# Performance work log

Measured on AMD Instinct MI355X. Metric: run time of the kernel, lower is better.

Reference implementation:

```python
import jax, jax.numpy as jnp
import numpy as np

B, L, F_DIM, H = 4, 384, 640, 128
K_COULOMB = 332.0
DIELECTRIC = 80.0
BN_EPS = 1e-5

# amino-acid charge table, index order 'ACDEFGHIKLMNPQRSTVWY'
_AA = 'ACDEFGHIKLMNPQRSTVWY'
_CHG = {'D': -1.0, 'E': -1.0, 'K': 1.0, 'R': 1.0, 'H': 0.1}
_TABLE = np.zeros((20, 3), dtype=np.float32)
for _i, _aa in enumerate(_AA):
    c = _CHG.get(_aa, 0.0)
    _TABLE[_i, 0 if c > 0 else (1 if c < 0 else 2)] = 1.0
CHG_TABLE = jnp.asarray(_TABLE)


def _conv1d(x, w, b, pad):
    # x: [N, Cin, L], w: [Cout, Cin, K]
    y = jax.lax.conv_general_dilated(x, w, (1,), [(pad, pad)],
                                     dimension_numbers=('NCH', 'OIH', 'NCH'))
    return y + b[None, :, None]


def setup_inputs() -> dict:
    key = jax.random.key(0)
    ks = jax.random.split(key, 32)
    s = 0.05

    def rn(k, shape):
        return (jax.random.normal(k, shape) * s).astype(jnp.float32)

    inp = {
        'features': jax.random.normal(ks[0], (B, L, F_DIM), dtype=jnp.float32),
        'seq_ids': jax.random.randint(ks[1], (B, L), 0, 20, dtype=jnp.int32),
        'structures': (jax.random.normal(ks[2], (B, L, 3)) * 10.0).astype(jnp.float32),
        # charge predictor: Linear(F,H) -> ReLU -> BN(H) -> Linear(H,H//2) -> ReLU -> Linear(H//2,3) -> Softmax
        'W1': rn(ks[3], (F_DIM, H)), 'b1': jnp.zeros((H,), jnp.float32),
        'gamma': jnp.ones((H,), jnp.float32), 'beta': jnp.zeros((H,), jnp.float32),
        'rmean': jnp.zeros((H,), jnp.float32), 'rvar': jnp.ones((H,), jnp.float32),
        'W2': rn(ks[4], (H, H // 2)), 'b2': jnp.zeros((H // 2,), jnp.float32),
        'W3': rn(ks[5], (H // 2, 3)), 'b3': jnp.zeros((3,), jnp.float32),
        # salt bridge detector: Linear(2F+1,H) -> ReLU -> Linear(H,64) -> ReLU -> Linear(64,1) -> Sigmoid
        'sW1': rn(ks[6], (2 * F_DIM + 1, H)), 'sb1': jnp.zeros((H,), jnp.float32),
        'sW2': rn(ks[7], (H, 64)), 'sb2': jnp.zeros((64,), jnp.float32),
        'sW3': rn(ks[8], (64, 1)), 'sb3': jnp.zeros((1,), jnp.float32),
        # potential calculator convs (OIH layout)
        'c1w': rn(ks[9], (16, 1, 5)), 'c1b': jnp.zeros((16,), jnp.float32),
        'c2w': rn(ks[10], (8, 16, 3)), 'c2b': jnp.zeros((8,), jnp.float32),
        'c3w': rn(ks[11], (1, 8, 3)), 'c3b': jnp.zeros((1,), jnp.float32),
    }
    return inp


def reference(features, seq_ids, structures,
              W1, b1, gamma, beta, rmean, rvar, W2, b2, W3, b3,
              sW1, sb1, sW2, sb2, sW3, sb3,
              c1w, c1b, c2w, c2b, c3w, c3b):
    b_, l_, f_ = features.shape

    # true charges from sequence (one-hot pos/neg/neutral)
    true_charges = CHG_TABLE[seq_ids]                               # [B,L,3]

    # --- charge predictor (BatchNorm in eval mode: running stats) ---
    x = features.reshape(-1, f_)
    h = jax.nn.relu(x @ W1 + b1)
    h = gamma * (h - rmean) / jnp.sqrt(rvar + BN_EPS) + beta
    h = jax.nn.relu(h @ W2 + b2)
    pc = jax.nn.softmax(h @ W3 + b3, axis=-1).reshape(b_, l_, 3)    # [B,L,3]

    net_charge = pc[:, :, 0:1] - pc[:, :, 1:2]                      # [B,L,1]

    # --- electrostatic potential: 1D conv stack on [B,1,L] ---
    p = net_charge.transpose(0, 2, 1)                               # [B,1,L]
    p = jax.nn.relu(_conv1d(p, c1w, c1b, 2))
    p = jax.nn.relu(_conv1d(p, c2w, c2b, 1))
    p = _conv1d(p, c3w, c3b, 1)
    potential = p.transpose(0, 2, 1)                                # [B,L,1]

    # --- pairwise distances ---
    diff = structures[:, :, None, :] - structures[:, None, :, :]    # [B,L,L,3]
    D = jnp.sqrt(jnp.sum(diff * diff, axis=-1) + 1e-12)             # [B,L,L]

    # --- salt bridges: vectorized edge-MLP over all (pos i, neg j) pairs ---
    pos = pc[:, :, 0] > pc[:, :, 2]                                 # [B,L]
    neg = pc[:, :, 1] > pc[:, :, 2]                                 # [B,L]
    a, bb, d = sW1[:f_], sW1[f_:2 * f_], sW1[2 * f_]                # split cat([fi,fj,dist]) @ sW1
    fi = features @ a                                               # [B,L,H]
    fj = features @ bb                                              # [B,L,H]
    hid = jax.nn.relu(fi[:, :, None, :] + fj[:, None, :, :] + D[..., None] * d + sb1)  # [B,L,L,H]
    hid2 = jax.nn.relu(hid @ sW2 + sb2)                             # [B,L,L,64]
    prob = jax.nn.sigmoid((hid2 @ sW3 + sb3)[..., 0])               # [B,L,L]
    q = pos[:, :, None] & neg[:, None, :] & (D < 4.0) & (prob > 0.5)
    salt_bridge_masks = (q | q.transpose(0, 2, 1)).astype(jnp.float32)  # [B,L,L]

    # --- Coulomb energy with distance-dependent dielectric ---
    # dielectric = eps * D / 4 -> e_ij = k * q_i q_j / (eps/4 * D^2)
    qc = pc[:, :, 0] - pc[:, :, 1]                                  # [B,L]
    valid = (D < 15.0) & (D > 0.0)
    triu = jnp.triu(jnp.ones((l_, l_), bool), k=1)[None]
    D_safe = jnp.where(valid, D, 1.0)
    e_ij = K_COULOMB * qc[:, :, None] * qc[:, None, :] / ((DIELECTRIC / 4.0) * D_safe * D_safe)
    energy = jnp.sum(jnp.where(valid & triu, e_ij, 0.0), axis=(1, 2))  # [B]

    return (pc, true_charges, net_charge, potential, salt_bridge_masks, energy)
```

## Files before the change

### kernel.cpp

```cpp
#include <hip/hip_runtime.h>

#define LSEQ 384
#define NROWS 1536
#define FDIM 640
#define HDIM 128
#define PART 196608

#define WS_H1P 0
#define WS_FIP (4*PART)
#define WS_FJP (8*PART)
#define WS_FI  (12*PART)
#define WS_FJ  (13*PART)
#define WS_QC  (14*PART)
#define WS_FLAG (WS_QC + NROWS)

#define OUT_PC    0
#define OUT_TC    4608
#define OUT_NET   9216
#define OUT_POT   10752
#define OUT_MASK  12288
#define OUT_EN    602112

__global__ __launch_bounds__(256) void k_gemm(const float* __restrict__ X,
                                              const float* __restrict__ W1,
                                              const float* __restrict__ sW1,
                                              float* __restrict__ ws,
                                              float* __restrict__ out) {
    __shared__ float As[2 * 32 * 34];
    __shared__ float Bs[2 * 32 * 64];
    const int t = threadIdx.x;
    if (blockIdx.x == 0 && blockIdx.y == 0 && blockIdx.z == 0 && t < 4)
        out[OUT_EN + t] = 0.0f;

    const int m0 = blockIdx.x * 32;
    const int gy = blockIdx.y, kz = blockIdx.z;
    const int mat = gy >> 1, half = gy & 1, n0 = half * 64;
    const float* W = (mat == 0) ? W1 : (mat == 1 ? sW1 : sW1 + 640 * 128);
    float* O = ws + (mat == 0 ? WS_H1P : (mat == 1 ? WS_FIP : WS_FJP)) + kz * PART;

    const int a_r = t >> 3, a_c = (t & 7) * 4;
    const int b_r = t >> 4, b_c = (t & 15) * 4;
    const int tx = (t & 15) * 4, ty = (t >> 4) * 2;
    const int k0 = kz * 160;

    float acc[2][4] = {};

    float4 av  = *(const float4*)&X[(m0 + a_r) * FDIM + k0 + a_c];
    float4 bv0 = *(const float4*)&W[(k0 + b_r) * HDIM + n0 + b_c];
    float4 bv1 = *(const float4*)&W[(k0 + b_r + 16) * HDIM + n0 + b_c];
    As[(a_c + 0) * 34 + a_r] = av.x;
    As[(a_c + 1) * 34 + a_r] = av.y;
    As[(a_c + 2) * 34 + a_r] = av.z;
    As[(a_c + 3) * 34 + a_r] = av.w;
    *(float4*)&Bs[b_r * 64 + b_c]        = bv0;
    *(float4*)&Bs[(b_r + 16) * 64 + b_c] = bv1;
    __syncthreads();

    for (int it = 0; it < 5; it++) {
        const int buf = it & 1;
        if (it < 4) {
            const int kk = k0 + (it + 1) * 32;
            av  = *(const float4*)&X[(m0 + a_r) * FDIM + kk + a_c];
            bv0 = *(const float4*)&W[(kk + b_r) * HDIM + n0 + b_c];
            bv1 = *(const float4*)&W[(kk + b_r + 16) * HDIM + n0 + b_c];
        }
        const float* Ab = As + buf * 1088;
        const float* Bb = Bs + buf * 2048;
#pragma unroll
        for (int k = 0; k < 32; k++) {
            float2 a = *(const float2*)&Ab[k * 34 + ty];
            float4 b = *(const float4*)&Bb[k * 64 + tx];
            acc[0][0] = fmaf(a.x, b.x, acc[0][0]);
            acc[0][1] = fmaf(a.x, b.y, acc[0][1]);
            acc[0][2] = fmaf(a.x, b.z, acc[0][2]);
            acc[0][3] = fmaf(a.x, b.w, acc[0][3]);
            acc[1][0] = fmaf(a.y, b.x, acc[1][0]);
            acc[1][1] = fmaf(a.y, b.y, acc[1][1]);
            acc[1][2] = fmaf(a.y, b.z, acc[1][2]);
            acc[1][3] = fmaf(a.y, b.w, acc[1][3]);
        }
        if (it < 4) {
            float* Aw = As + (buf ^ 1) * 1088;
            float* Bw = Bs + (buf ^ 1) * 2048;
            Aw[(a_c + 0) * 34 + a_r] = av.x;
            Aw[(a_c + 1) * 34 + a_r] = av.y;
            Aw[(a_c + 2) * 34 + a_r] = av.z;
            Aw[(a_c + 3) * 34 + a_r] = av.w;
            *(float4*)&Bw[b_r * 64 + b_c]        = bv0;
            *(float4*)&Bw[(b_r + 16) * 64 + b_c] = bv1;
            __syncthreads();
        }
    }
#pragma unroll
    for (int r = 0; r < 2; r++) {
        float4 v = make_float4(acc[r][0], acc[r][1], acc[r][2], acc[r][3]);
        *(float4*)&O[(m0 + ty + r) * HDIM + n0 + tx] = v;
    }
}

__global__ __launch_bounds__(256) void k_row(float* __restrict__ ws,
                                             const float* __restrict__ b1,
                                             const float* __restrict__ gam,
                                             const float* __restrict__ bet,
                                             const float* __restrict__ rmean,
                                             const float* __restrict__ rvar,
                                             const float* __restrict__ W2,
                                             const float* __restrict__ b2,
                                             const float* __restrict__ W3,
                                             const float* __restrict__ b3,
                                             const int* __restrict__ seq,
                                             float* __restrict__ out) {
    const int t = threadIdx.x, w = t >> 6, lane = t & 63;
    const int row = blockIdx.x * 4 + w;
    const long base = (long)row * 128;
    const float* h1p = ws + WS_H1P;
    const float* fip = ws + WS_FIP;
    const float* fjp = ws + WS_FJP;

    {
        float fi0 = fip[base + lane] + fip[PART + base + lane]
                  + fip[2 * PART + base + lane] + fip[3 * PART + base + lane];
        float fi1 = fip[base + 64 + lane] + fip[PART + base + 64 + lane]
                  + fip[2 * PART + base + 64 + lane] + fip[3 * PART + base + 64 + lane];
        float fj0 = fjp[base + lane] + fjp[PART + base + lane]
                  + fjp[2 * PART + base + lane] + fjp[3 * PART + base + lane];
        float fj1 = fjp[base + 64 + lane] + fjp[PART + base + 64 + lane]
                  + fjp[2 * PART + base + 64 + lane] + fjp[3 * PART + base + 64 + lane];
        ws[WS_FI + base + lane]      = fi0;
        ws[WS_FI + base + 64 + lane] = fi1;
        ws[WS_FJ + base + lane]      = fj0;
        ws[WS_FJ + base + 64 + lane] = fj1;
    }

    float h0 = h1p[base + lane] + h1p[PART + base + lane]
             + h1p[2 * PART + base + lane] + h1p[3 * PART + base + lane];
    float h1 = h1p[base + 64 + lane] + h1p[PART + base + 64 + lane]
             + h1p[2 * PART + base + 64 + lane] + h1p[3 * PART + base + 64 + lane];
    h0 = fmaxf(h0 + b1[lane], 0.0f);
    h1 = fmaxf(h1 + b1[64 + lane], 0.0f);
    h0 = gam[lane]      * (h0 - rmean[lane])      / sqrtf(rvar[lane] + 1e-5f)      + bet[lane];
    h1 = gam[64 + lane] * (h1 - rmean[64 + lane]) / sqrtf(rvar[64 + lane] + 1e-5f) + bet[64 + lane];

    float acc = b2[lane];
#pragma unroll
    for (int cc = 0; cc < 64; cc++) {
        float wv0 = W2[cc * 64 + lane];
        float wv1 = W2[(cc + 64) * 64 + lane];
        float hv0 = __uint_as_float(__builtin_amdgcn_readlane(__float_as_uint(h0), cc));
        float hv1 = __uint_as_float(__builtin_amdgcn_readlane(__float_as_uint(h1), cc));
        acc = fmaf(hv0, wv0, acc);
        acc = fmaf(hv1, wv1, acc);
    }
    float h2 = fmaxf(acc, 0.0f);
    float x0 = h2 * W3[lane * 3 + 0];
    float x1 = h2 * W3[lane * 3 + 1];
    float x2 = h2 * W3[lane * 3 + 2];
#pragma unroll
    for (int o = 32; o > 0; o >>= 1) {
        x0 += __shfl_xor(x0, o, 64);
        x1 += __shfl_xor(x1, o, 64);
        x2 += __shfl_xor(x2, o, 64);
    }
    if (lane == 0) {
        float l0 = x0 + b3[0], l1 = x1 + b3[1], l2 = x2 + b3[2];
        float m = fmaxf(l0, fmaxf(l1, l2));
        float e0 = expf(l0 - m), e1 = expf(l1 - m), e2 = expf(l2 - m);
        float s = e0 + e1 + e2;
        float pc0 = e0 / s, pc1 = e1 / s, pc2 = e2 / s;
        out[OUT_PC + row * 3 + 0] = pc0;
        out[OUT_PC + row * 3 + 1] = pc1;
        out[OUT_PC + row * 3 + 2] = pc2;
        float net = pc0 - pc1;
        out[OUT_NET + row] = net;
        ws[WS_QC + row] = net;
        ((int*)(ws + WS_FLAG))[row] = (pc0 > pc2 ? 1 : 0) | (pc1 > pc2 ? 2 : 0);
        int sid = seq[row];
        float c0 = (sid == 6 || sid == 8 || sid == 14) ? 1.0f : 0.0f;
        float c1 = (sid == 2 || sid == 3) ? 1.0f : 0.0f;
        out[OUT_TC + row * 3 + 0] = c0;
        out[OUT_TC + row * 3 + 1] = c1;
        out[OUT_TC + row * 3 + 2] = (c0 == 0.0f && c1 == 0.0f) ? 1.0f : 0.0f;
    }
}

__device__ __forceinline__ float mlp_eval(const float* __restrict__ fi, const float* __restrict__ fj,
                                          int gi, int gj, float D,
                                          float dv0, float dv1, float sb0, float sb1v,
                                          float b2v, float w3l, const float* w2s, int lane) {
    float fi0 = fi[(long)gi * 128 + lane];
    float fi1 = fi[(long)gi * 128 + 64 + lane];
    float fj0 = fj[(long)gj * 128 + lane];
    float fj1 = fj[(long)gj * 128 + 64 + lane];
    float h0 = fmaxf(fi0 + fj0 + D * dv0 + sb0, 0.0f);
    float h1 = fmaxf(fi1 + fj1 + D * dv1 + sb1v, 0.0f);
    float a0 = 0.0f, a1 = 0.0f;
#pragma unroll
    for (int cc = 0; cc < 64; cc++) {
        float hv0 = __uint_as_float(__builtin_amdgcn_readlane(__float_as_uint(h0), cc));
        float hv1 = __uint_as_float(__builtin_amdgcn_readlane(__float_as_uint(h1), cc));
        a0 = fmaf(hv0, w2s[cc * 64 + lane], a0);
        a1 = fmaf(hv1, w2s[(cc + 64) * 64 + lane], a1);
    }
    float x = fmaxf(a0 + a1 + b2v, 0.0f) * w3l;
#pragma unroll
    for (int o = 32; o > 0; o >>= 1) x += __shfl_xor(x, o, 64);
    return x;
}

__global__ __launch_bounds__(256) void k2(const float* __restrict__ S,
                                          const float* __restrict__ ws,
                                          const float* __restrict__ sW1,
                                          const float* __restrict__ sb1,
                                          const float* __restrict__ sW2,
                                          const float* __restrict__ sb2,
                                          const float* __restrict__ sW3,
                                          const float* __restrict__ sb3,
                                          const float* __restrict__ c1w, const float* __restrict__ c1b,
                                          const float* __restrict__ c2w, const float* __restrict__ c2b,
                                          const float* __restrict__ c3w, const float* __restrict__ c3b,
                                          float* __restrict__ out) {
    __shared__ char smem[40960];
    const int t = threadIdx.x;
    const int bi = blockIdx.x;

    if (bi < 4) {
        float* p0 = (float*)smem;
        float* p1 = p0 + 388;
        float* p2 = p1 + 16 * 386;
        const int b = bi;
        for (int j = t; j < LSEQ; j += 256) p0[j + 2] = out[OUT_NET + b * LSEQ + j];
        if (t < 2) { p0[t] = 0.0f; p0[LSEQ + 2 + t] = 0.0f; }
        if (t < 16) { p1[t * 386] = 0.0f; p1[t * 386 + 385] = 0.0f; }
        if (t < 8)  { p2[t * 386] = 0.0f; p2[t * 386 + 385] = 0.0f; }
        __syncthreads();
        for (int pos = t; pos < LSEQ; pos += 256) {
#pragma unroll
            for (int o = 0; o < 16; o++) {
                float acc = c1b[o];
#pragma unroll
                for (int k = 0; k < 5; k++) acc = fmaf(p0[pos + k], c1w[o * 5 + k], acc);
                p1[o * 386 + pos + 1] = fmaxf(acc, 0.0f);
            }
        }
        __syncthreads();
        for (int pos = t; pos < LSEQ; pos += 256) {
#pragma unroll
            for (int o = 0; o < 8; o++) {
                float acc = c2b[o];
                for (int i = 0; i < 16; i++)
#pragma unroll
                    for (int k = 0; k < 3; k++)
                        acc = fmaf(p1[i * 386 + pos + k], c2w[(o * 16 + i) * 3 + k], acc);
                p2[o * 386 + pos + 1] = fmaxf(acc, 0.0f);
            }
        }
        __syncthreads();
        for (int pos = t; pos < LSEQ; pos += 256) {
            float acc = c3b[0];
            for (int i = 0; i < 8; i++)
#pragma unroll
                for (int k = 0; k < 3; k++)
                    acc = fmaf(p2[i * 386 + pos + k], c3w[i * 3 + k], acc);
            out[OUT_POT + b * LSEQ + pos] = acc;
        }
        return;
    }

    float* sx = (float*)smem;
    float* sy = sx + 384;
    float* sz = sy + 384;
    float* sq = sz + 384;
    unsigned int* clist = (unsigned int*)(sz + 768);
    unsigned char* sf = (unsigned char*)(smem + 7680);
    float* red = (float*)(smem + 8064);
    int* cntL = (int*)(smem + 8080);
    float* w2s = (float*)(smem + 8192);

    const float* qc = ws + WS_QC;
    const int* flags = (const int*)(ws + WS_FLAG);
    const float* fi = ws + WS_FI;
    const float* fj = ws + WS_FJ;

    const int row = bi - 4;
    const int b = row / LSEQ;
    const int i = row - b * LSEQ;

    for (int j = t; j < LSEQ; j += 256) {
        int g = b * LSEQ + j;
        sx[j] = S[g * 3 + 0];
        sy[j] = S[g * 3 + 1];
        sz[j] = S[g * 3 + 2];
        sq[j] = qc[g];
        sf[j] = (unsigned char)flags[g];
    }
    if (t == 0) *cntL = 0;
    __syncthreads();

    const float six = sx[i], siy = sy[i], siz = sz[i], qi = sq[i];
    const int fli = sf[i];
    const bool posi = (fli & 1) != 0, negi = (fli & 2) != 0;
    const int lane = t & 63, w = t >> 6;
    float esum = 0.0f;
    float* mrow = out + OUT_MASK + (long)row * LSEQ;

    for (int j = t; j < LSEQ; j += 256) {
        float dx = __fsub_rn(six, sx[j]);
        float dy = __fsub_rn(siy, sy[j]);
        float dz = __fsub_rn(siz, sz[j]);
        float d2 = __fadd_rn(__fadd_rn(__fmul_rn(dx, dx), __fmul_rn(dy, dy)), __fmul_rn(dz, dz));
        d2 = __fadd_rn(d2, 1e-12f);
        float D = __fsqrt_rn(d2);
        mrow[j] = 0.0f;
        if (j > i && D < 15.0f && D > 0.0f) {
            float num = __fmul_rn(__fmul_rn(332.0f, qi), sq[j]);
            float den = __fmul_rn(__fmul_rn(20.0f, D), D);
            esum += __fdiv_rn(num, den);
        }
        int flj = sf[j];
        bool near = (D < 4.0f);
        bool need1 = near && posi && ((flj & 2) != 0);
        bool need2 = near && negi && ((flj & 1) != 0);
        if (need1 || need2) {
            int p = atomicAdd(cntL, 1);
            clist[p] = (unsigned int)j | (need1 ? 512u : 0u) | (need2 ? 1024u : 0u);
        }
    }
#pragma unroll
    for (int o = 32; o > 0; o >>= 1) esum += __shfl_xor(esum, o, 64);
    if (lane == 0) red[w] = esum;
    __syncthreads();
    if (t == 0) {
        float s = red[0] + red[1] + red[2] + red[3];
        atomicAdd(&out[OUT_EN + b], s);
    }

    int nc = *cntL;
    if (nc == 0) return;

    for (int idx = t; idx < 2048; idx += 256)
        ((float4*)w2s)[idx] = ((const float4*)sW2)[idx];
    const float* dvec = sW1 + 1280 * 128;
    const float dv0 = dvec[lane], dv1 = dvec[lane + 64];
    const float sb0 = sb1[lane], sb1v = sb1[lane + 64];
    const float w3l = sW3[lane];
    const float b2v = sb2[lane];
    const float b3v = sb3[0];
    __syncthreads();

    for (int c = w; c < nc; c += 4) {
        unsigned int e = clist[c];
        int j = (int)(e & 511u);
        bool need1 = (e & 512u) != 0, need2 = (e & 1024u) != 0;
        float dx = __fsub_rn(six, sx[j]);
        float dy = __fsub_rn(siy, sy[j]);
        float dz = __fsub_rn(siz, sz[j]);
        float d2 = __fadd_rn(__fadd_rn(__fmul_rn(dx, dx), __fmul_rn(dy, dy)), __fmul_rn(dz, dz));
        d2 = __fadd_rn(d2, 1e-12f);
        float D = __fsqrt_rn(d2);
        int gi = row, gj = b * LSEQ + j;
        bool hit = false;
        if (need1) {
            float x = mlp_eval(fi, fj, gi, gj, D, dv0, dv1, sb0, sb1v, b2v, w3l, w2s, lane);
            hit = (x + b3v) > 0.0f;
        }
        if (!hit && need2) {
            float x = mlp_eval(fi, fj, gj, gi, D, dv0, dv1, sb0, sb1v, b2v, w3l, w2s, lane);
            hit = (x + b3v) > 0.0f;
        }
        if (hit && lane == 0) mrow[j] = 1.0f;
    }
}

extern "C" void kernel_launch(void* const* d_in, const int* in_sizes, int n_in,
                              void* d_out, int out_size, void* d_ws, size_t ws_size,
                              hipStream_t stream) {
    const float* X     = (const float*)d_in[0];
    const int*   seq   = (const int*)d_in[1];
    const float* S     = (const float*)d_in[2];
    const float* W1    = (const float*)d_in[3];
    const float* b1    = (const float*)d_in[4];
    const float* gam   = (const float*)d_in[5];
    const float* bet   = (const float*)d_in[6];
    const float* rmean = (const float*)d_in[7];
    const float* rvar  = (const float*)d_in[8];
    const float* W2    = (const float*)d_in[9];
    const float* b2    = (const float*)d_in[10];
    const float* W3    = (const float*)d_in[11];
    const float* b3    = (const float*)d_in[12];
    const float* sW1   = (const float*)d_in[13];
    const float* sb1   = (const float*)d_in[14];
    const float* sW2   = (const float*)d_in[15];
    const float* sb2   = (const float*)d_in[16];
    const float* sW3   = (const float*)d_in[17];
    const float* sb3   = (const float*)d_in[18];
    const float* c1w   = (const float*)d_in[19];
    const float* c1b   = (const float*)d_in[20];
    const float* c2w   = (const float*)d_in[21];
    const float* c2b   = (const float*)d_in[22];
    const float* c3w   = (const float*)d_in[23];
    const float* c3b   = (const float*)d_in[24];

    float* out = (float*)d_out;
    float* ws  = (float*)d_ws;

    hipLaunchKernelGGL(k_gemm, dim3(48, 6, 4), dim3(256), 0, stream, X, W1, sW1, ws, out);
    hipLaunchKernelGGL(k_row, dim3(384), dim3(256), 0, stream,
                       ws, b1, gam, bet, rmean, rvar, W2, b2, W3, b3, seq, out);
    hipLaunchKernelGGL(k2, dim3(1540), dim3(256), 0, stream,
                       S, ws, sW1, sb1, sW2, sb2, sW3, sb3,
                       c1w, c1b, c2w, c2b, c3w, c3b, out);
}
```

Measured before the change: 155.8 us.

## Shrink k2 shared memory, fuse conv chain in registers, spread energy reduction

Cuts k2's shared memory from 40KB to 8KB. The salt-bridge MLP now reads sW2 straight from global/L2 instead of staging it in LDS, and the launch bounds hint 6 blocks per CU to raise occupancy. The three potential convolutions are fused per position into register computation, recomputing the conv1 and conv2 halos instead of keeping intermediate LDS buffers. Energy accumulation now spreads atomics over 96 partial slots per batch, and the last block to finish does the final reduction. This avoids contended atomics on four output words but adds a completion counter and the cost of global-memory weight reads.

New measurement: 168.7 us. 8.3% more time.

```diff
diff --git a/kernel.cpp b/kernel.cpp
--- a/kernel.cpp
+++ b/kernel.cpp
@@ -13,6 +13,8 @@
 #define WS_FJ  (13*PART)
 #define WS_QC  (14*PART)
 #define WS_FLAG (WS_QC + NROWS)
+#define WS_EPART (WS_FLAG + NROWS)
+#define WS_DONE  (WS_EPART + 384)
 
 #define OUT_PC    0
 #define OUT_TC    4608
@@ -24,13 +26,14 @@
 __global__ __launch_bounds__(256) void k_gemm(const float* __restrict__ X,
                                               const float* __restrict__ W1,
                                               const float* __restrict__ sW1,
-                                              float* __restrict__ ws,
-                                              float* __restrict__ out) {
+                                              float* __restrict__ ws) {
     __shared__ float As[2 * 32 * 34];
     __shared__ float Bs[2 * 32 * 64];
     const int t = threadIdx.x;
-    if (blockIdx.x == 0 && blockIdx.y == 0 && blockIdx.z == 0 && t < 4)
-        out[OUT_EN + t] = 0.0f;
+    if (blockIdx.x == 0 && blockIdx.y == 0 && blockIdx.z == 0) {
+        for (int idx = t; idx < 385; idx += 256)
+            ws[WS_EPART + idx] = 0.0f;
+    }
 
     const int m0 = blockIdx.x * 32;
     const int gy = blockIdx.y, kz = blockIdx.z;
@@ -186,20 +189,16 @@
 __device__ __forceinline__ float mlp_eval(const float* __restrict__ fi, const float* __restrict__ fj,
                                           int gi, int gj, float D,
                                           float dv0, float dv1, float sb0, float sb1v,
-                                          float b2v, float w3l, const float* w2s, int lane) {
-    float fi0 = fi[(long)gi * 128 + lane];
-    float fi1 = fi[(long)gi * 128 + 64 + lane];
-    float fj0 = fj[(long)gj * 128 + lane];
-    float fj1 = fj[(long)gj * 128 + 64 + lane];
-    float h0 = fmaxf(fi0 + fj0 + D * dv0 + sb0, 0.0f);
-    float h1 = fmaxf(fi1 + fj1 + D * dv1 + sb1v, 0.0f);
+                                          float b2v, float w3l, const float* __restrict__ sW2, int lane) {
+    float h0 = fmaxf(fi[(long)gi * 128 + lane]      + fj[(long)gj * 128 + lane]      + D * dv0 + sb0,  0.0f);
+    float h1 = fmaxf(fi[(long)gi * 128 + 64 + lane] + fj[(long)gj * 128 + 64 + lane] + D * dv1 + sb1v, 0.0f);
     float a0 = 0.0f, a1 = 0.0f;
-#pragma unroll
+#pragma unroll 8
     for (int cc = 0; cc < 64; cc++) {
         float hv0 = __uint_as_float(__builtin_amdgcn_readlane(__float_as_uint(h0), cc));
         float hv1 = __uint_as_float(__builtin_amdgcn_readlane(__float_as_uint(h1), cc));
-        a0 = fmaf(hv0, w2s[cc * 64 + lane], a0);
-        a1 = fmaf(hv1, w2s[(cc + 64) * 64 + lane], a1);
+        a0 = fmaf(hv0, sW2[cc * 64 + lane], a0);
+        a1 = fmaf(hv1, sW2[(cc + 64) * 64 + lane], a1);
     }
     float x = fmaxf(a0 + a1 + b2v, 0.0f) * w3l;
 #pragma unroll
@@ -207,61 +206,68 @@
     return x;
 }
 
-__global__ __launch_bounds__(256) void k2(const float* __restrict__ S,
-                                          const float* __restrict__ ws,
-                                          const float* __restrict__ sW1,
-                                          const float* __restrict__ sb1,
-                                          const float* __restrict__ sW2,
-                                          const float* __restrict__ sb2,
-                                          const float* __restrict__ sW3,
-                                          const float* __restrict__ sb3,
-                                          const float* __restrict__ c1w, const float* __restrict__ c1b,
-                                          const float* __restrict__ c2w, const float* __restrict__ c2b,
-                                          const float* __restrict__ c3w, const float* __restrict__ c3b,
-                                          float* __restrict__ out) {
-    __shared__ char smem[40960];
+__global__ __launch_bounds__(256, 6) void k2(const float* __restrict__ S,
+                                             float* __restrict__ ws,
+                                             const float* __restrict__ sW1,
+                                             const float* __restrict__ sb1,
+                                             const float* __restrict__ sW2,
+                                             const float* __restrict__ sb2,
+                                             const float* __restrict__ sW3,
+                                             const float* __restrict__ sb3,
+                                             const float* __restrict__ c1w, const float* __restrict__ c1b,
+                                             const float* __restrict__ c2w, const float* __restrict__ c2b,
+                                             const float* __restrict__ c3w, const float* __restrict__ c3b,
+                                             float* __restrict__ out) {
+    __shared__ char smem[8192];
     const int t = threadIdx.x;
     const int bi = blockIdx.x;
 
     if (bi < 4) {
-        float* p0 = (float*)smem;
-        float* p1 = p0 + 388;
-        float* p2 = p1 + 16 * 386;
+        float* p0h = (float*)smem;
         const int b = bi;
-        for (int j = t; j < LSEQ; j += 256) p0[j + 2] = out[OUT_NET + b * LSEQ + j];
-        if (t < 2) { p0[t] = 0.0f; p0[LSEQ + 2 + t] = 0.0f; }
-        if (t < 16) { p1[t * 386] = 0.0f; p1[t * 386 + 385] = 0.0f; }
-        if (t < 8)  { p2[t * 386] = 0.0f; p2[t * 386 + 385] = 0.0f; }
+        for (int idx = t; idx < 392; idx += 256)
+            p0h[idx] = (idx >= 4 && idx < 388) ? out[OUT_NET + b * LSEQ + (idx - 4)] : 0.0f;
         __syncthreads();
         for (int pos = t; pos < LSEQ; pos += 256) {
-#pragma unroll
-            for (int o = 0; o < 16; o++) {
-                float acc = c1b[o];
-#pragma unroll
-                for (int k = 0; k < 5; k++) acc = fmaf(p0[pos + k], c1w[o * 5 + k], acc);
-                p1[o * 386 + pos + 1] = fmaxf(acc, 0.0f);
-            }
-        }
-        __syncthreads();
-        for (int pos = t; pos < LSEQ; pos += 256) {
-#pragma unroll
-            for (int o = 0; o < 8; o++) {
-                float acc = c2b[o];
-                for (int i = 0; i < 16; i++)
-#pragma unroll
-                    for (int k = 0; k < 3; k++)
-                        acc = fmaf(p1[i * 386 + pos + k], c2w[(o * 16 + i) * 3 + k], acc);
-                p2[o * 386 + pos + 1] = fmaxf(acc, 0.0f);
-            }
-        }
-        __syncthreads();
-        for (int pos = t; pos < LSEQ; pos += 256) {
-            float acc = c3b[0];
-            for (int i = 0; i < 8; i++)
-#pragma unroll
-                for (int k = 0; k < 3; k++)
-                    acc = fmaf(p2[i * 386 + pos + k], c3w[i * 3 + k], acc);
-            out[OUT_POT + b * LSEQ + pos] = acc;
+            float p2v[8][3];
+#pragma unroll
+            for (int o2 = 0; o2 < 8; o2++) {
+                float cb = c2b[o2];
+#pragma unroll
+                for (int d1 = 0; d1 < 3; d1++) p2v[o2][d1] = cb;
+            }
+            for (int i = 0; i < 16; i++) {
+                float p1v[5];
+#pragma unroll
+                for (int d2 = 0; d2 < 5; d2++) {
+                    int q2 = pos - 2 + d2;
+                    float a = c1b[i];
+#pragma unroll
+                    for (int k = 0; k < 5; k++)
+                        a = fmaf(p0h[q2 + 2 + k], c1w[i * 5 + k], a);
+                    p1v[d2] = (q2 >= 0 && q2 < LSEQ) ? fmaxf(a, 0.0f) : 0.0f;
+                }
+#pragma unroll
+                for (int o2 = 0; o2 < 8; o2++) {
+#pragma unroll
+                    for (int d1 = 0; d1 < 3; d1++) {
+#pragma unroll
+                        for (int k = 0; k < 3; k++)
+                            p2v[o2][d1] = fmaf(p1v[d1 + k], c2w[(o2 * 16 + i) * 3 + k], p2v[o2][d1]);
+                    }
+                }
+            }
+            float acc3 = c3b[0];
+#pragma unroll
+            for (int o2 = 0; o2 < 8; o2++) {
+#pragma unroll
+                for (int k = 0; k < 3; k++) {
+                    int q1 = pos - 1 + k;
+                    float pv = (q1 >= 0 && q1 < LSEQ) ? fmaxf(p2v[o2][k], 0.0f) : 0.0f;
+                    acc3 = fmaf(pv, c3w[o2 * 3 + k], acc3);
+                }
+            }
+            out[OUT_POT + b * LSEQ + pos] = acc3;
         }
         return;
     }
@@ -270,11 +276,10 @@
     float* sy = sx + 384;
     float* sz = sy + 384;
     float* sq = sz + 384;
-    unsigned int* clist = (unsigned int*)(sz + 768);
+    unsigned int* clist = (unsigned int*)(sq + 384);
     unsigned char* sf = (unsigned char*)(smem + 7680);
     float* red = (float*)(smem + 8064);
     int* cntL = (int*)(smem + 8080);
-    float* w2s = (float*)(smem + 8192);
 
     const float* qc = ws + WS_QC;
     const int* flags = (const int*)(ws + WS_FLAG);
@@ -329,45 +334,59 @@
     for (int o = 32; o > 0; o >>= 1) esum += __shfl_xor(esum, o, 64);
     if (lane == 0) red[w] = esum;
     __syncthreads();
+
+    int nc = *cntL;
+    float blockE = red[0] + red[1] + red[2] + red[3];
+
+    if (nc > 0) {
+        const float* dvec = sW1 + 1280 * 128;
+        const float dv0 = dvec[lane], dv1 = dvec[lane + 64];
+        const float sb0 = sb1[lane], sb1v = sb1[lane + 64];
+        const float w3l = sW3[lane];
+        const float b2v = sb2[lane];
+        const float b3v = sb3[0];
+        for (int c = w; c < nc; c += 4) {
+            unsigned int e = clist[c];
+            int j = (int)(e & 511u);
+            bool need1 = (e & 512u) != 0, need2 = (e & 1024u) != 0;
+            float dx = __fsub_rn(six, sx[j]);
+            float dy = __fsub_rn(siy, sy[j]);
+            float dz = __fsub_rn(siz, sz[j]);
+            float d2 = __fadd_rn(__fadd_rn(__fmul_rn(dx, dx), __fmul_rn(dy, dy)), __fmul_rn(dz, dz));
+            d2 = __fadd_rn(d2, 1e-12f);
+            float D = __fsqrt_rn(d2);
+            int gi = row, gj = b * LSEQ + j;
+            bool hit = false;
+            if (need1) {
+                float x = mlp_eval(fi, fj, gi, gj, D, dv0, dv1, sb0, sb1v, b2v, w3l, sW2, lane);
+                hit = (x + b3v) > 0.0f;
+            }
+            if (!hit && need2) {
+                float x = mlp_eval(fi, fj, gj, gi, D, dv0, dv1, sb0, sb1v, b2v, w3l, sW2, lane);
+                hit = (x + b3v) > 0.0f;
+            }
+            if (hit && lane == 0) mrow[j] = 1.0f;
+        }
+    }
+
+    unsigned int old = 0xffffffffu;
     if (t == 0) {
-        float s = red[0] + red[1] + red[2] + red[3];
-        atomicAdd(&out[OUT_EN + b], s);
-    }
-
-    int nc = *cntL;
-    if (nc == 0) return;
-
-    for (int idx = t; idx < 2048; idx += 256)
-        ((float4*)w2s)[idx] = ((const float4*)sW2)[idx];
-    const float* dvec = sW1 + 1280 * 128;
-    const float dv0 = dvec[lane], dv1 = dvec[lane + 64];
-    const float sb0 = sb1[lane], sb1v = sb1[lane + 64];
-    const float w3l = sW3[lane];
-    const float b2v = sb2[lane];
-    const float b3v = sb3[0];
-    __syncthreads();
-
-    for (int c = w; c < nc; c += 4) {
-        unsigned int e = clist[c];
-        int j = (int)(e & 511u);
-        bool need1 = (e & 512u) != 0, need2 = (e & 1024u) != 0;
-        float dx = __fsub_rn(six, sx[j]);
-        float dy = __fsub_rn(siy, sy[j]);
-        float dz = __fsub_rn(siz, sz[j]);
-        float d2 = __fadd_rn(__fadd_rn(__fmul_rn(dx, dx), __fmul_rn(dy, dy)), __fmul_rn(dz, dz));
-        d2 = __fadd_rn(d2, 1e-12f);
-        float D = __fsqrt_rn(d2);
-        int gi = row, gj = b * LSEQ + j;
-        bool hit = false;
-        if (need1) {
-            float x = mlp_eval(fi, fj, gi, gj, D, dv0, dv1, sb0, sb1v, b2v, w3l, w2s, lane);
-            hit = (x + b3v) > 0.0f;
-        }
-        if (!hit && need2) {
-            float x = mlp_eval(fi, fj, gj, gi, D, dv0, dv1, sb0, sb1v, b2v, w3l, w2s, lane);
-            hit = (x + b3v) > 0.0f;
-        }
-        if (hit && lane == 0) mrow[j] = 1.0f;
+        atomicAdd(&ws[WS_EPART + b * 96 + (i % 96)], blockE);
+        __threadfence();
+        old = atomicAdd((unsigned int*)&ws[WS_DONE], 1u);
+    }
+    if (t < 64) {
+        old = __shfl(old, 0, 64);
+        if (old == (unsigned int)(NROWS - 1)) {
+#pragma unroll
+            for (int bb = 0; bb < 4; bb++) {
+                float s = ws[WS_EPART + bb * 96 + lane];
+                if (lane < 32) s += ws[WS_EPART + bb * 96 + 64 + lane];
+#pragma unroll
+                for (int o = 32; o > 0; o >>= 1) s += __shfl_xor(s, o, 64);
+                if (lane == 0) out[OUT_EN + bb] = s;
+            }
+        }
     }
 }
 
@@ -403,7 +422,7 @@
     float* out = (float*)d_out;
     float* ws  = (float*)d_ws;
 
-    hipLaunchKernelGGL(k_gemm, dim3(48, 6, 4), dim3(256), 0, stream, X, W1, sW1, ws, out);
+    hipLaunchKernelGGL(k_gemm, dim3(48, 6, 4), dim3(256), 0, stream, X, W1, sW1, ws);
     hipLaunchKernelGGL(k_row, dim3(384), dim3(256), 0, stream,
                        ws, b1, gam, bet, rmean, rvar, W2, b2, W3, b3, seq, out);
     hipLaunchKernelGGL(k2, dim3(1540), dim3(256), 0, stream,
```
